# Performance work log

Hardware: AMD Instinct MI355X
Metric: run time of the kernel (lower is better)

## Reference

```python
import jax, jax.numpy as jnp
import numpy as np

DT = 0.001  # seconds per step (keras_spiking default)
BATCH, SEQ, SIZE = 64, 1024, 512


def setup_inputs() -> dict:
    key = jax.random.key(0)
    k1, k2 = jax.random.split(key)
    inputs = jax.random.normal(k1, (BATCH, SEQ, SIZE), dtype=jnp.float32)
    initial_level = jnp.zeros((SIZE,), dtype=jnp.float32)
    # time constants around the 0.01s used in the docstring example
    tau = 0.005 + 0.05 * jax.random.uniform(k2, (SIZE,), dtype=jnp.float32)
    return {"inputs": inputs, "initial_level": initial_level, "tau": tau}


def _alpha_filter(inputs, initial_level, tau):
    # inputs: [B, T, K]; initial_level, tau: [K]
    B_, T, K = inputs.shape
    tau_c = jnp.maximum(tau, 1e-8)               # clip for stability (as in forward pass)
    dt_tau = DT / tau_c                           # [K]
    dt_tau2 = dt_tau / tau_c                      # [K]
    e = jnp.exp(-dt_tau)                          # [K]
    # per-feature 2x2 transition matrix A: [K, 2, 2]
    row0 = jnp.stack([1.0 - dt_tau, -dt_tau2], axis=-1)             # [K, 2]
    row1 = jnp.stack([DT * jnp.ones_like(tau_c), 1.0 + dt_tau], -1)  # [K, 2]
    A = e[:, None, None] * jnp.stack([row0, row1], axis=-2)          # [K, 2, 2]
    # input vector B: [K, 2]
    Bvec = jnp.stack([e * dt_tau2, 1.0 - e * (1.0 + dt_tau)], axis=-1)
    Bt = Bvec.T  # [2, K]
    # initial state: row 0 zeros, row 1 initial_level -> [B, 2, K]
    x0 = jnp.stack(
        [jnp.zeros((B_, K), inputs.dtype),
         jnp.broadcast_to(initial_level, (B_, K))], axis=1)

    def step(x, u):
        # x: [B, 2, K], u: [B, K]
        xn = jnp.einsum('kij,mjk->mik', A, x) + Bt[None, :, :] * u[:, None, :]
        return xn, xn[:, 1]  # output is second state component

    _, ys = jax.lax.scan(step, x0, jnp.swapaxes(inputs, 0, 1))  # ys: [T, B, K]
    return jnp.swapaxes(ys, 0, 1)  # [B, T, K]


def reference(inputs, initial_level, tau):
    return _alpha_filter(inputs, initial_level, tau)
```

## Files before the change

### kernel.cpp

```cpp
#include <hip/hip_runtime.h>
#include <math.h>

namespace {
constexpr int kB  = 64;
constexpr int kT  = 1024;
constexpr int kK  = 512;
constexpr int kC  = 32;
constexpr int kL  = kT / kC;
constexpr int kKB = 32;
constexpr int kBlockThreads = kKB * kC;
constexpr float kDT = 0.001f;
}

__global__ __launch_bounds__(kBlockThreads, 8) void alpha_scan_c32(
    const float* __restrict__ in,
    const float* __restrict__ init_level,
    const float* __restrict__ tau,
    float* __restrict__ out)
{
    __shared__ float sx0[kC][kKB];
    __shared__ float sx1[kC][kKB];

    const int tid = threadIdx.x;
    const int kl  = tid & (kKB - 1);
    const int c   = tid >> 5;
    const int bx  = blockIdx.x;
    const int b   = bx >> 4;
    const int k   = ((bx & 15) << 5) + kl;

    const float tc      = fmaxf(tau[k], 1e-8f);
    const float dt_tau  = kDT / tc;
    const float dt_tau2 = dt_tau / tc;
    const float e       = expf(-dt_tau);

    const float a00 = e * (1.0f - dt_tau);
    const float a01 = e * (-dt_tau2);
    const float a10 = e * kDT;
    const float a11 = e * (1.0f + dt_tau);
    const float b0  = e * dt_tau2;
    const float b1  = 1.0f - e * (1.0f + dt_tau);

    const float il = init_level[k];

    const size_t base = (size_t)b * kT * kK + (size_t)c * kL * kK + k;
    const float* __restrict__ pin = in + base;

    float r[kL];
    #pragma unroll
    for (int i = 0; i < kL; ++i) r[i] = pin[(size_t)i * kK];

    float x0 = 0.0f, x1 = 0.0f;
    #pragma unroll
    for (int i = 0; i < kL; ++i) {
        const float u   = r[i];
        const float nx0 = fmaf(a00, x0, fmaf(a01, x1, b0 * u));
        const float nx1 = fmaf(a10, x0, fmaf(a11, x1, b1 * u));
        x0 = nx0; x1 = nx1;
        r[i] = nx1;
    }

    sx0[c][kl] = x0;
    sx1[c][kl] = x1;
    __syncthreads();

    float m00 = a00, m01 = a01, m10 = a10, m11 = a11;
    #pragma unroll
    for (int s = 0; s < 5; ++s) {
        const float t00 = fmaf(m00, m00, m01 * m10);
        const float t01 = fmaf(m00, m01, m01 * m11);
        const float t10 = fmaf(m10, m00, m11 * m10);
        const float t11 = fmaf(m10, m01, m11 * m11);
        m00 = t00; m01 = t01; m10 = t10; m11 = t11;
    }

    float v0 = 0.0f, v1 = il;
    for (int j = 0; j < c; ++j) {
        const float p0 = fmaf(m00, v0, m01 * v1) + sx0[j][kl];
        const float p1 = fmaf(m10, v0, m11 * v1) + sx1[j][kl];
        v0 = p0; v1 = p1;
    }

    float* __restrict__ pout = out + base;
    #pragma unroll
    for (int i = 0; i < kL; ++i) {
        const float n0 = fmaf(a00, v0, a01 * v1);
        const float n1 = fmaf(a10, v0, a11 * v1);
        v0 = n0; v1 = n1;
        pout[(size_t)i * kK] = r[i] + n1;
    }
}

extern "C" void kernel_launch(void* const* d_in, const int* in_sizes, int n_in,
                              void* d_out, int out_size, void* d_ws, size_t ws_size,
                              hipStream_t stream) {
    const float* in  = (const float*)d_in[0];
    const float* il  = (const float*)d_in[1];
    const float* tau = (const float*)d_in[2];
    float* out = (float*)d_out;

    dim3 block(kBlockThreads);
    dim3 grid(kB * (kK / kKB));
    alpha_scan_c32<<<grid, block, 0, stream>>>(in, il, tau, out);
}
```

Before: 248.4 us.

## Re-read inputs and rescan chunks instead of caching all chunk values in registers

Halves the number of time chunks per block (32 to 16), so each thread handles 64 steps, and no longer keeps the whole chunk's partial results in registers. The first pass streams inputs through a 16-entry rolling register buffer to get the chunk-end state. After the cross-chunk combine, the second pass reloads the inputs and rescans from the corrected carry-in state, writing outputs directly. This cuts register pressure and improves occupancy, but reads the input twice from memory (likely from L2/cache) and makes the sequential recurrence per thread longer.

```diff
diff --git a/kernel.cpp b/kernel.cpp
--- a/kernel.cpp
+++ b/kernel.cpp
@@ -5,14 +5,15 @@
 constexpr int kB  = 64;
 constexpr int kT  = 1024;
 constexpr int kK  = 512;
-constexpr int kC  = 32;
+constexpr int kC  = 16;
 constexpr int kL  = kT / kC;
 constexpr int kKB = 32;
 constexpr int kBlockThreads = kKB * kC;
+constexpr int kR  = 16;
 constexpr float kDT = 0.001f;
 }
 
-__global__ __launch_bounds__(kBlockThreads, 8) void alpha_scan_c32(
+__global__ __launch_bounds__(kBlockThreads, 8) void alpha_rescan(
     const float* __restrict__ in,
     const float* __restrict__ init_level,
     const float* __restrict__ tau,
@@ -45,18 +46,29 @@
     const size_t base = (size_t)b * kT * kK + (size_t)c * kL * kK + k;
     const float* __restrict__ pin = in + base;
 
-    float r[kL];
+    float buf[kR];
     #pragma unroll
-    for (int i = 0; i < kL; ++i) r[i] = pin[(size_t)i * kK];
+    for (int i = 0; i < kR; ++i) buf[i] = pin[(size_t)i * kK];
 
     float x0 = 0.0f, x1 = 0.0f;
     #pragma unroll
-    for (int i = 0; i < kL; ++i) {
-        const float u   = r[i];
+    for (int tb = 0; tb < kL - kR; tb += kR) {
+        const float* __restrict__ pld = pin + (size_t)(tb + kR) * kK;
+        #pragma unroll
+        for (int i = 0; i < kR; ++i) {
+            const float u = buf[i];
+            buf[i] = pld[(size_t)i * kK];
+            const float nx0 = fmaf(a00, x0, fmaf(a01, x1, b0 * u));
+            const float nx1 = fmaf(a10, x0, fmaf(a11, x1, b1 * u));
+            x0 = nx0; x1 = nx1;
+        }
+    }
+    #pragma unroll
+    for (int i = 0; i < kR; ++i) {
+        const float u = buf[i];
         const float nx0 = fmaf(a00, x0, fmaf(a01, x1, b0 * u));
         const float nx1 = fmaf(a10, x0, fmaf(a11, x1, b1 * u));
         x0 = nx0; x1 = nx1;
-        r[i] = nx1;
     }
 
     sx0[c][kl] = x0;
@@ -65,7 +77,7 @@
 
     float m00 = a00, m01 = a01, m10 = a10, m11 = a11;
     #pragma unroll
-    for (int s = 0; s < 5; ++s) {
+    for (int s = 0; s < 6; ++s) {
         const float t00 = fmaf(m00, m00, m01 * m10);
         const float t01 = fmaf(m00, m01, m01 * m11);
         const float t10 = fmaf(m10, m00, m11 * m10);
@@ -82,11 +94,32 @@
 
     float* __restrict__ pout = out + base;
     #pragma unroll
-    for (int i = 0; i < kL; ++i) {
-        const float n0 = fmaf(a00, v0, a01 * v1);
-        const float n1 = fmaf(a10, v0, a11 * v1);
-        v0 = n0; v1 = n1;
-        pout[(size_t)i * kK] = r[i] + n1;
+    for (int i = 0; i < kR; ++i) buf[i] = pin[(size_t)i * kK];
+
+    #pragma unroll
+    for (int tb = 0; tb < kL - kR; tb += kR) {
+        const float* __restrict__ pld = pin  + (size_t)(tb + kR) * kK;
+        float* __restrict__ pst       = pout + (size_t)tb * kK;
+        #pragma unroll
+        for (int i = 0; i < kR; ++i) {
+            const float u = buf[i];
+            buf[i] = pld[(size_t)i * kK];
+            const float n0 = fmaf(a00, v0, fmaf(a01, v1, b0 * u));
+            const float n1 = fmaf(a10, v0, fmaf(a11, v1, b1 * u));
+            v0 = n0; v1 = n1;
+            pst[(size_t)i * kK] = n1;
+        }
+    }
+    {
+        float* __restrict__ pst = pout + (size_t)(kL - kR) * kK;
+        #pragma unroll
+        for (int i = 0; i < kR; ++i) {
+            const float u = buf[i];
+            const float n0 = fmaf(a00, v0, fmaf(a01, v1, b0 * u));
+            const float n1 = fmaf(a10, v0, fmaf(a11, v1, b1 * u));
+            v0 = n0; v1 = n1;
+            pst[(size_t)i * kK] = n1;
+        }
     }
 }
 
@@ -100,5 +133,5 @@
 
     dim3 block(kBlockThreads);
     dim3 grid(kB * (kK / kKB));
-    alpha_scan_c32<<<grid, block, 0, stream>>>(in, il, tau, out);
+    alpha_rescan<<<grid, block, 0, stream>>>(in, il, tau, out);
 }
```

Result: slower. 340.0 us (+36.9%).
